# Kernel optimization log

Hardware: AMD Instinct MI355X
Metric: run time of the kernel (lower is better)

## Reference

```python
import jax, jax.numpy as jnp
import numpy as np


def setup_inputs() -> dict:
    key = jax.random.key(0)
    k1, k2, k3 = jax.random.split(key, 3)
    dim = 192
    x = jax.random.normal(k1, (4, dim, 256, 256), dtype=jnp.float32)
    # Conv2d(5*dim, dim, 1): weight [dim, 5*dim], bias [dim]
    W = jax.random.normal(k2, (dim, 5 * dim), dtype=jnp.float32) * 0.02
    b = jax.random.normal(k3, (dim,), dtype=jnp.float32) * 0.02
    return {"x": x, "W": W, "b": b}


def _shifts(x):
    # Matches torch: cat([x,
    #   pad(x[:,:,:,1:], (0,1)),   # take right neighbor (zero at last col)
    #   pad(x[:,:,:,:-1], (1,0)),  # take left neighbor (zero at first col)
    #   pad(x[:,:,1:,:], (0,0,0,1)),  # take below neighbor (zero at last row)
    #   pad(x[:,:,:-1,:], (0,0,1,0))  # take above neighbor (zero at first row)
    # ], dim=1)
    right = jnp.pad(x[:, :, :, 1:], ((0, 0), (0, 0), (0, 0), (0, 1)))
    left = jnp.pad(x[:, :, :, :-1], ((0, 0), (0, 0), (0, 0), (1, 0)))
    down = jnp.pad(x[:, :, 1:, :], ((0, 0), (0, 0), (0, 1), (0, 0)))
    up = jnp.pad(x[:, :, :-1, :], ((0, 0), (0, 0), (1, 0), (0, 0)))
    return jnp.concatenate([x, right, left, down, up], axis=1)  # [B, 5C, H, W]


def reference(x, W, b):
    xs = _shifts(x)  # [B, 5C, H, W]
    # 1x1 conv == per-pixel matmul over channels
    out = jnp.einsum("bchw,oc->bohw", xs, W) + b[None, :, None, None]
    return out
```

## Files before the change

### kernel.cpp

```cpp
#include <hip/hip_runtime.h>
#include <hip/hip_bf16.h>
#include <stdint.h>

#define CDIM 192
#define KDIM 960
#define HW   65536
#define WI   256

#define OFF_W    50331648u
#define OFF_BIAS 50700288u
#define OFF_FLAG 50701056u
#define NEED_TOTAL 50701120u

typedef __attribute__((ext_vector_type(8))) short short8;
typedef __attribute__((ext_vector_type(4))) float floatx4;

__device__ __forceinline__ uint16_t f2b(float v) {
    __hip_bfloat16 h = __float2bfloat16(v);
    return *reinterpret_cast<uint16_t*>(&h);
}

__global__ __launch_bounds__(256) void detect_kernel(const uint32_t* __restrict__ xw,
                                                     int* __restrict__ flag) {
    __shared__ int cnt;
    if (threadIdx.x == 0) cnt = 0;
    __syncthreads();
    int local = 0;
    #pragma unroll
    for (int i = 0; i < 4; ++i) {
        int s = threadIdx.x * 4 + i;
        uint32_t d = xw[(size_t)s * 24571];
        uint32_t e = (d >> 7) & 0xFF;
        if (e >= 110 && e <= 130) ++local;
    }
    atomicAdd(&cnt, local);
    __syncthreads();
    if (threadIdx.x == 0) *flag = (cnt >= 512) ? 1 : 0;
}

__global__ __launch_bounds__(256) void prep_kernel(const void* __restrict__ Wsrc,
                                                   const void* __restrict__ bsrc,
                                                   __hip_bfloat16* __restrict__ Wb,
                                                   float* __restrict__ bfp,
                                                   const int* __restrict__ flag) {
    const int f = *flag;
    if (blockIdx.x < 720) {
        int i = blockIdx.x * 256 + threadIdx.x;
        float v = f ? __bfloat162float(((const __hip_bfloat16*)Wsrc)[i])
                    : ((const float*)Wsrc)[i];
        Wb[i] = __float2bfloat16(v);
    } else if (threadIdx.x < CDIM) {
        int j = threadIdx.x;
        bfp[j] = f ? __bfloat162float(((const __hip_bfloat16*)bsrc)[j])
                   : ((const float*)bsrc)[j];
    }
}

__global__ __launch_bounds__(256) void transpose_kernel(const void* __restrict__ xsrc,
                                                        __hip_bfloat16* __restrict__ xt,
                                                        const int* __restrict__ flag,
                                                        int base_b) {
    __shared__ uint4 lds[1536];
    const int bid = blockIdx.x;
    const int tid = threadIdx.x;
    const int bb = bid >> 10;
    const int b  = base_b + bb;
    const int p0 = (bid & 1023) << 6;
    const int f = *flag;
    if (f) {
        const uint4* xg = (const uint4*)xsrc;
        #pragma unroll
        for (int it = 0; it < 6; ++it) {
            int idx = tid + it * 256;
            int c = idx >> 3, pxc = idx & 7;
            size_t off = (size_t)(b * CDIM + c) * HW + p0 + pxc * 8;
            lds[idx] = xg[off >> 3];
        }
    } else {
        const float4* xg = (const float4*)xsrc;
        #pragma unroll
        for (int it = 0; it < 6; ++it) {
            int idx = tid + it * 256;
            int c = idx >> 3, pxc = idx & 7;
            size_t off4 = ((size_t)(b * CDIM + c) * HW + p0 + pxc * 8) >> 2;
            float4 v0 = xg[off4], v1 = xg[off4 + 1];
            uint32_t w0 = f2b(v0.x) | ((uint32_t)f2b(v0.y) << 16);
            uint32_t w1 = f2b(v0.z) | ((uint32_t)f2b(v0.w) << 16);
            uint32_t w2 = f2b(v1.x) | ((uint32_t)f2b(v1.y) << 16);
            uint32_t w3 = f2b(v1.z) | ((uint32_t)f2b(v1.w) << 16);
            lds[idx] = make_uint4(w0, w1, w2, w3);
        }
    }
    __syncthreads();
    const uint16_t* lu = (const uint16_t*)lds;
    #pragma unroll
    for (int it = 0; it < 6; ++it) {
        int idx = tid + it * 256;
        int px = idx & 63, cc = idx >> 6;
        uint32_t d[4];
        #pragma unroll
        for (int w = 0; w < 4; ++w) {
            uint32_t lo = lu[(cc * 8 + 2 * w) * 64 + px];
            uint32_t hi = lu[(cc * 8 + 2 * w + 1) * 64 + px];
            d[w] = lo | (hi << 16);
        }
        size_t row = (size_t)bb * HW + p0 + px;
        *(uint4*)(xt + row * CDIM + cc * 8) = make_uint4(d[0], d[1], d[2], d[3]);
    }
}

__device__ __forceinline__ void gload16(const void* g, void* l) {
    __builtin_amdgcn_global_load_lds(
        (const __attribute__((address_space(1))) uint32_t*)g,
        (__attribute__((address_space(3))) uint32_t*)l, 16, 0, 0);
}

__global__ __launch_bounds__(256, 2) void gemm_kernel(const __hip_bfloat16* __restrict__ xt,
                                                      const __hip_bfloat16* __restrict__ Wm,
                                                      const float* __restrict__ biasf,
                                                      void* __restrict__ outv,
                                                      const int* __restrict__ flag,
                                                      int base_b) {
    __shared__ char ldsW[2 * 12288];
    const int f = *flag;
    const int tid  = threadIdx.x;
    const int lane = tid & 63, wave = tid >> 6;
    const int quad = lane >> 4, l15 = lane & 15;
    const int bid = blockIdx.x;
    const int bb = bid >> 9;
    const int b  = base_b + bb;
    const int r  = bid & 511;
    const int h  = r >> 1;
    const int w0 = (r & 1) << 7;
    const int p0 = h * WI + w0;
    const int obase = (wave >> 1) * 96;
    const int nbase = (wave & 1) * 64;

    const char* gw[3];
    int ldsoff[3];
    #pragma unroll
    for (int t = 0; t < 3; ++t) {
        int chunk = tid + t * 256;
        int kq = chunk / 192, o = chunk % 192;
        gw[t] = (const char*)Wm + ((size_t)o * KDIM + kq * 8) * 2;
        ldsoff[t] = chunk * 16;
    }
    int aoff[6];
    #pragma unroll
    for (int mt = 0; mt < 6; ++mt) {
        int o = obase + mt * 16 + l15;
        aoff[mt] = (quad * 192 + o) * 16;
    }
    const char* xb = (const char*)(xt + (size_t)bb * HW * CDIM);
    int prow[4]; bool w255[4], wzero[4];
    #pragma unroll
    for (int nt = 0; nt < 4; ++nt) {
        int pl = nbase + nt * 16 + l15;
        prow[nt]  = p0 + pl;
        w255[nt]  = ((w0 + pl) == 255);
        wzero[nt] = ((w0 + pl) == 0);
    }

    floatx4 acc[6][4];
    #pragma unroll
    for (int mt = 0; mt < 6; ++mt)
        #pragma unroll
        for (int nt = 0; nt < 4; ++nt)
            acc[mt][nt] = (floatx4){0.f, 0.f, 0.f, 0.f};

    #pragma unroll
    for (int t = 0; t < 3; ++t) gload16(gw[t], ldsW + ldsoff[t]);

    for (int s = 0; s < 5; ++s) {
        const int dp = (s == 0) ? 0 : (s == 1) ? 1 : (s == 2) ? -1 : (s == 3) ? WI : -WI;
        const bool skip = (s == 3 && h == 255) || (s == 4 && h == 0);
        const int dpe = skip ? 0 : dp;
        #pragma unroll
        for (int j6 = 0; j6 < 6; ++j6) {
            const int step = s * 6 + j6;
            __syncthreads();
            const int cur = (step & 1) * 12288;
            if (step < 29) {
                const int nxt = ((step + 1) & 1) * 12288;
                #pragma unroll
                for (int t = 0; t < 3; ++t)
                    gload16(gw[t] + (size_t)(step + 1) * 64, ldsW + nxt + ldsoff[t]);
            }
            short8 af[6];
            #pragma unroll
            for (int mt = 0; mt < 6; ++mt)
                af[mt] = *(const short8*)(ldsW + cur + aoff[mt]);
            short8 bf[4];
            #pragma unroll
            for (int nt = 0; nt < 4; ++nt) {
                const bool edge = (s == 1 && w255[nt]) || (s == 2 && wzero[nt]);
                int rowi = prow[nt] + dpe;
                if (edge) rowi = prow[nt];
                short8 v = *(const short8*)(xb +
                    ((size_t)rowi * CDIM + j6 * 32 + quad * 8) * 2);
                if (edge || skip)
                    v = (short8){0, 0, 0, 0, 0, 0, 0, 0};
                bf[nt] = v;
            }
            #pragma unroll
            for (int mt = 0; mt < 6; ++mt)
                #pragma unroll
                for (int nt = 0; nt < 4; ++nt)
                    acc[mt][nt] = __builtin_amdgcn_mfma_f32_16x16x32_bf16(
                        af[mt], bf[nt], acc[mt][nt], 0, 0, 0);
        }
    }

    #pragma unroll
    for (int mt = 0; mt < 6; ++mt) {
        int o0 = obase + mt * 16 + quad * 4;
        float bv[4];
        #pragma unroll
        for (int rr = 0; rr < 4; ++rr) bv[rr] = biasf[o0 + rr];
        #pragma unroll
        for (int nt = 0; nt < 4; ++nt) {
            int px = nbase + nt * 16 + l15;
            size_t base = ((size_t)(b * CDIM + o0) * HW) + p0 + px;
            if (f) {
                __hip_bfloat16* out = (__hip_bfloat16*)outv;
                #pragma unroll
                for (int rr = 0; rr < 4; ++rr)
                    out[base + (size_t)rr * HW] = __float2bfloat16(acc[mt][nt][rr] + bv[rr]);
            } else {
                float* out = (float*)outv;
                #pragma unroll
                for (int rr = 0; rr < 4; ++rr)
                    out[base + (size_t)rr * HW] = acc[mt][nt][rr] + bv[rr];
            }
        }
    }
}

__global__ __launch_bounds__(256) void fallback_kernel(const void* __restrict__ xv,
                                                       const void* __restrict__ Wv,
                                                       const void* __restrict__ bv,
                                                       void* __restrict__ outv,
                                                       const int* __restrict__ flag) {
    __shared__ float Wl[KDIM];
    const int f = *flag;
    const int tid = threadIdx.x;
    const int bid = blockIdx.x;
    const int h = bid & 255;
    const int bo = bid >> 8;
    const int o = bo % CDIM;
    const int b = bo / CDIM;
    if (f) {
        const __hip_bfloat16* W16 = (const __hip_bfloat16*)Wv;
        for (int i = tid; i < KDIM; i += 256) Wl[i] = __bfloat162float(W16[(size_t)o * KDIM + i]);
    } else {
        const float* W32 = (const float*)Wv;
        for (int i = tid; i < KDIM; i += 256) Wl[i] = W32[(size_t)o * KDIM + i];
    }
    __syncthreads();
    const size_t pb = (size_t)b * CDIM * HW + (size_t)h * WI + tid;
    float acc = f ? __bfloat162float(((const __hip_bfloat16*)bv)[o]) : ((const float*)bv)[o];
    if (f) {
        const __hip_bfloat16* x = (const __hip_bfloat16*)xv;
        for (int c = 0; c < CDIM; ++c) {
            const __hip_bfloat16* xp = x + pb + (size_t)c * HW;
            float ctr = __bfloat162float(xp[0]);
            float rgt = (tid < 255) ? __bfloat162float(xp[1])   : 0.f;
            float lft = (tid > 0)   ? __bfloat162float(xp[-1])  : 0.f;
            float dwn = (h < 255)   ? __bfloat162float(xp[WI])  : 0.f;
            float up  = (h > 0)     ? __bfloat162float(xp[-WI]) : 0.f;
            acc += ctr * Wl[c] + rgt * Wl[192 + c] + lft * Wl[384 + c]
                 + dwn * Wl[576 + c] + up * Wl[768 + c];
        }
    } else {
        const float* x = (const float*)xv;
        for (int c = 0; c < CDIM; ++c) {
            const float* xp = x + pb + (size_t)c * HW;
            float ctr = xp[0];
            float rgt = (tid < 255) ? xp[1]   : 0.f;
            float lft = (tid > 0)   ? xp[-1]  : 0.f;
            float dwn = (h < 255)   ? xp[WI]  : 0.f;
            float up  = (h > 0)     ? xp[-WI] : 0.f;
            acc += ctr * Wl[c] + rgt * Wl[192 + c] + lft * Wl[384 + c]
                 + dwn * Wl[576 + c] + up * Wl[768 + c];
        }
    }
    size_t oidx = (size_t)bo * HW + (size_t)h * WI + tid;
    if (f) ((__hip_bfloat16*)outv)[oidx] = __float2bfloat16(acc);
    else   ((float*)outv)[oidx] = acc;
}

extern "C" void kernel_launch(void* const* d_in, const int* in_sizes, int n_in,
                              void* d_out, int out_size, void* d_ws, size_t ws_size,
                              hipStream_t stream) {
    const uint32_t* xw = (const uint32_t*)d_in[0];
    char* ws = (char*)d_ws;

    if (ws_size >= NEED_TOTAL) {
        int* flag = (int*)(ws + OFF_FLAG);
        __hip_bfloat16* xt = (__hip_bfloat16*)ws;
        __hip_bfloat16* Wb = (__hip_bfloat16*)(ws + OFF_W);
        float* bfp = (float*)(ws + OFF_BIAS);
        detect_kernel<<<1, 256, 0, stream>>>(xw, flag);
        prep_kernel<<<721, 256, 0, stream>>>(d_in[1], d_in[2], Wb, bfp, flag);
        for (int rnd = 0; rnd < 2; ++rnd) {
            transpose_kernel<<<2048, 256, 0, stream>>>(d_in[0], xt, flag, 2 * rnd);
            gemm_kernel<<<1024, 256, 0, stream>>>(xt, Wb, bfp, d_out, flag, 2 * rnd);
        }
    } else {
        int* flag = (int*)ws;
        detect_kernel<<<1, 256, 0, stream>>>(xw, flag);
        fallback_kernel<<<4 * CDIM * 256, 256, 0, stream>>>(d_in[0], d_in[1], d_in[2],
                                                            d_out, flag);
    }
}
```

Baseline: 573.6 us.

## Fuse transpose into GEMM by staging shifted input rows in LDS

Removes the separate transpose kernel and the bf16 transposed workspace. The fused kernel loads three input rows (h-1, h, h+1) for each 32-channel slice straight from the original NCHW tensor, converts them to bf16 and stores them in LDS with halo columns. The five shifted operands are then read from LDS, so input is fetched once per slice instead of five times from global memory. It also remaps workgroup IDs, adds explicit waitcnt/barrier scheduling and raises priority around the MFMA block. The cost is extra LDS use and per-slice synchronisation, plus strided global loads of 2 bytes per element in the staging step.

```diff
diff --git a/kernel.cpp b/kernel.cpp
--- a/kernel.cpp
+++ b/kernel.cpp
@@ -7,10 +7,14 @@
 #define HW   65536
 #define WI   256
 
-#define OFF_W    50331648u
-#define OFF_BIAS 50700288u
-#define OFF_FLAG 50701056u
-#define NEED_TOTAL 50701120u
+#define OFF_BIAS 368640u
+#define OFF_FLAG 369408u
+#define NEED_WS  369472u
+
+#define ROW_B    80
+#define SLICE_B  10560
+#define WOFF     31680
+#define WBUF     12288
 
 typedef __attribute__((ext_vector_type(8))) short short8;
 typedef __attribute__((ext_vector_type(4))) float floatx4;
@@ -56,80 +60,31 @@
     }
 }
 
-__global__ __launch_bounds__(256) void transpose_kernel(const void* __restrict__ xsrc,
-                                                        __hip_bfloat16* __restrict__ xt,
-                                                        const int* __restrict__ flag,
-                                                        int base_b) {
-    __shared__ uint4 lds[1536];
-    const int bid = blockIdx.x;
-    const int tid = threadIdx.x;
-    const int bb = bid >> 10;
-    const int b  = base_b + bb;
-    const int p0 = (bid & 1023) << 6;
-    const int f = *flag;
-    if (f) {
-        const uint4* xg = (const uint4*)xsrc;
-        #pragma unroll
-        for (int it = 0; it < 6; ++it) {
-            int idx = tid + it * 256;
-            int c = idx >> 3, pxc = idx & 7;
-            size_t off = (size_t)(b * CDIM + c) * HW + p0 + pxc * 8;
-            lds[idx] = xg[off >> 3];
-        }
-    } else {
-        const float4* xg = (const float4*)xsrc;
-        #pragma unroll
-        for (int it = 0; it < 6; ++it) {
-            int idx = tid + it * 256;
-            int c = idx >> 3, pxc = idx & 7;
-            size_t off4 = ((size_t)(b * CDIM + c) * HW + p0 + pxc * 8) >> 2;
-            float4 v0 = xg[off4], v1 = xg[off4 + 1];
-            uint32_t w0 = f2b(v0.x) | ((uint32_t)f2b(v0.y) << 16);
-            uint32_t w1 = f2b(v0.z) | ((uint32_t)f2b(v0.w) << 16);
-            uint32_t w2 = f2b(v1.x) | ((uint32_t)f2b(v1.y) << 16);
-            uint32_t w3 = f2b(v1.z) | ((uint32_t)f2b(v1.w) << 16);
-            lds[idx] = make_uint4(w0, w1, w2, w3);
-        }
-    }
-    __syncthreads();
-    const uint16_t* lu = (const uint16_t*)lds;
-    #pragma unroll
-    for (int it = 0; it < 6; ++it) {
-        int idx = tid + it * 256;
-        int px = idx & 63, cc = idx >> 6;
-        uint32_t d[4];
-        #pragma unroll
-        for (int w = 0; w < 4; ++w) {
-            uint32_t lo = lu[(cc * 8 + 2 * w) * 64 + px];
-            uint32_t hi = lu[(cc * 8 + 2 * w + 1) * 64 + px];
-            d[w] = lo | (hi << 16);
-        }
-        size_t row = (size_t)bb * HW + p0 + px;
-        *(uint4*)(xt + row * CDIM + cc * 8) = make_uint4(d[0], d[1], d[2], d[3]);
-    }
-}
-
 __device__ __forceinline__ void gload16(const void* g, void* l) {
     __builtin_amdgcn_global_load_lds(
         (const __attribute__((address_space(1))) uint32_t*)g,
         (__attribute__((address_space(3))) uint32_t*)l, 16, 0, 0);
 }
 
-__global__ __launch_bounds__(256, 2) void gemm_kernel(const __hip_bfloat16* __restrict__ xt,
-                                                      const __hip_bfloat16* __restrict__ Wm,
-                                                      const float* __restrict__ biasf,
-                                                      void* __restrict__ outv,
-                                                      const int* __restrict__ flag,
-                                                      int base_b) {
-    __shared__ char ldsW[2 * 12288];
+__global__ __launch_bounds__(256, 2) void fused_kernel(const void* __restrict__ xsrc,
+                                                       const __hip_bfloat16* __restrict__ Wm,
+                                                       const float* __restrict__ biasf,
+                                                       void* __restrict__ outv,
+                                                       const int* __restrict__ flag) {
+    __shared__ char lds[WOFF + 2 * WBUF];
+    char* xsl  = lds;
+    char* ldsW = lds + WOFF;
     const int f = *flag;
     const int tid  = threadIdx.x;
     const int lane = tid & 63, wave = tid >> 6;
     const int quad = lane >> 4, l15 = lane & 15;
-    const int bid = blockIdx.x;
-    const int bb = bid >> 9;
-    const int b  = base_b + bb;
-    const int r  = bid & 511;
+
+    const int nwg  = (int)gridDim.x;
+    const int bid0 = (int)blockIdx.x;
+    const int wg   = (bid0 & 7) * (nwg >> 3) + (bid0 >> 3);
+
+    const int bb = wg >> 9;
+    const int r  = wg & 511;
     const int h  = r >> 1;
     const int w0 = (r & 1) << 7;
     const int p0 = h * WI + w0;
@@ -151,14 +106,33 @@
         int o = obase + mt * 16 + l15;
         aoff[mt] = (quad * 192 + o) * 16;
     }
-    const char* xb = (const char*)(xt + (size_t)bb * HW * CDIM);
-    int prow[4]; bool w255[4], wzero[4];
+
+    int pxa[4]; bool w255[4], wzero[4];
     #pragma unroll
     for (int nt = 0; nt < 4; ++nt) {
         int pl = nbase + nt * 16 + l15;
-        prow[nt]  = p0 + pl;
+        pxa[nt]   = (pl + 1) * ROW_B;
         w255[nt]  = ((w0 + pl) == 255);
         wzero[nt] = ((w0 + pl) == 0);
+    }
+
+    const int scc  = tid >> 7;
+    const int spx  = (tid & 127) + 1;
+    const int scol = w0 + (tid & 127);
+    const int ec = tid >> 1, ee = tid & 1;
+    int ecol = ee ? (w0 + 128) : (w0 - 1);
+    if (ecol < 0) ecol = 0;
+    if (ecol > 255) ecol = 255;
+    const int epx = ee ? 129 : 0;
+
+    const size_t esz = f ? 2u : 4u;
+    const char* xp = (const char*)xsrc + (size_t)bb * CDIM * HW * esz;
+
+    int hr[3];
+    #pragma unroll
+    for (int rr = 0; rr < 3; ++rr) {
+        int v = h - 1 + rr;
+        hr[rr] = v < 0 ? 0 : (v > 255 ? 255 : v);
     }
 
     floatx4 acc[6][4];
@@ -168,46 +142,100 @@
         for (int nt = 0; nt < 4; ++nt)
             acc[mt][nt] = (floatx4){0.f, 0.f, 0.f, 0.f};
 
+#define STAGE(JJ)                                                                          \
+    {                                                                                      \
+        const int c0 = (JJ) * 32;                                                          \
+        _Pragma("unroll")                                                                  \
+        for (int rr = 0; rr < 3; ++rr) {                                                   \
+            uint32_t tmp[16];                                                              \
+            const size_t rowoff = (size_t)hr[rr] * WI;                                     \
+            if (f) {                                                                       \
+                const uint16_t* xg = (const uint16_t*)xp;                                  \
+                _Pragma("unroll")                                                          \
+                for (int cc = 0; cc < 16; ++cc)                                            \
+                    tmp[cc] = xg[(size_t)(c0 + scc * 16 + cc) * HW + rowoff + scol];       \
+            } else {                                                                       \
+                const float* xg = (const float*)xp;                                        \
+                _Pragma("unroll")                                                          \
+                for (int cc = 0; cc < 16; ++cc)                                            \
+                    tmp[cc] = f2b(xg[(size_t)(c0 + scc * 16 + cc) * HW + rowoff + scol]);  \
+            }                                                                              \
+            uint4 q0, q1;                                                                  \
+            q0.x = tmp[0] | (tmp[1] << 16);  q0.y = tmp[2] | (tmp[3] << 16);               \
+            q0.z = tmp[4] | (tmp[5] << 16);  q0.w = tmp[6] | (tmp[7] << 16);               \
+            q1.x = tmp[8] | (tmp[9] << 16);  q1.y = tmp[10] | (tmp[11] << 16);             \
+            q1.z = tmp[12] | (tmp[13] << 16); q1.w = tmp[14] | (tmp[15] << 16);            \
+            char* base = xsl + rr * SLICE_B + spx * ROW_B + scc * 32;                      \
+            *(uint4*)(base)      = q0;                                                     \
+            *(uint4*)(base + 16) = q1;                                                     \
+        }                                                                                  \
+        if (tid < 64) {                                                                    \
+            _Pragma("unroll")                                                              \
+            for (int rr = 0; rr < 3; ++rr) {                                               \
+                const size_t gi = (size_t)(c0 + ec) * HW + (size_t)hr[rr] * WI + ecol;     \
+                uint16_t v = f ? ((const uint16_t*)xp)[gi]                                 \
+                               : f2b(((const float*)xp)[gi]);                              \
+                *(uint16_t*)(xsl + rr * SLICE_B + epx * ROW_B + ec * 2) = v;               \
+            }                                                                              \
+        }                                                                                  \
+    }
+
     #pragma unroll
     for (int t = 0; t < 3; ++t) gload16(gw[t], ldsW + ldsoff[t]);
-
-    for (int s = 0; s < 5; ++s) {
-        const int dp = (s == 0) ? 0 : (s == 1) ? 1 : (s == 2) ? -1 : (s == 3) ? WI : -WI;
-        const bool skip = (s == 3 && h == 255) || (s == 4 && h == 0);
-        const int dpe = skip ? 0 : dp;
+    STAGE(0)
+    __syncthreads();
+
+    for (int j = 0; j < 6; ++j) {
         #pragma unroll
-        for (int j6 = 0; j6 < 6; ++j6) {
-            const int step = s * 6 + j6;
-            __syncthreads();
-            const int cur = (step & 1) * 12288;
-            if (step < 29) {
-                const int nxt = ((step + 1) & 1) * 12288;
+        for (int s = 0; s < 5; ++s) {
+            const int cur = (s & 1) * WBUF;
+            __builtin_amdgcn_s_barrier();
+            __builtin_amdgcn_sched_barrier(0);
+            if (s < 4) {
+                const int nxt = WBUF - cur;
                 #pragma unroll
                 for (int t = 0; t < 3; ++t)
-                    gload16(gw[t] + (size_t)(step + 1) * 64, ldsW + nxt + ldsoff[t]);
+                    gload16(gw[t] + (size_t)((s + 1) * 6 + j) * 64, ldsW + nxt + ldsoff[t]);
             }
+            __builtin_amdgcn_sched_barrier(0);
+            if (s < 4) asm volatile("s_waitcnt vmcnt(3)" ::: "memory");
+            else       asm volatile("s_waitcnt vmcnt(0)" ::: "memory");
+            __builtin_amdgcn_sched_barrier(0);
+            __builtin_amdgcn_s_barrier();
+            __builtin_amdgcn_sched_barrier(0);
+
             short8 af[6];
             #pragma unroll
             for (int mt = 0; mt < 6; ++mt)
                 af[mt] = *(const short8*)(ldsW + cur + aoff[mt]);
+
+            const int so   = (s == 3) ? 2 * SLICE_B : (s == 4) ? 0 : SLICE_B;
+            const int dw80 = (s == 1) ? ROW_B : (s == 2) ? -ROW_B : 0;
+            const bool skip = (s == 3 && h == 255) || (s == 4 && h == 0);
             short8 bf[4];
             #pragma unroll
             for (int nt = 0; nt < 4; ++nt) {
-                const bool edge = (s == 1 && w255[nt]) || (s == 2 && wzero[nt]);
-                int rowi = prow[nt] + dpe;
-                if (edge) rowi = prow[nt];
-                short8 v = *(const short8*)(xb +
-                    ((size_t)rowi * CDIM + j6 * 32 + quad * 8) * 2);
-                if (edge || skip)
-                    v = (short8){0, 0, 0, 0, 0, 0, 0, 0};
-                bf[nt] = v;
+                short8 v = *(const short8*)(xsl + so + pxa[nt] + dw80 + quad * 16);
+                const bool kill = skip || (s == 1 && w255[nt]) || (s == 2 && wzero[nt]);
+                bf[nt] = kill ? (short8){0, 0, 0, 0, 0, 0, 0, 0} : v;
             }
+
+            __builtin_amdgcn_s_setprio(1);
             #pragma unroll
             for (int mt = 0; mt < 6; ++mt)
                 #pragma unroll
                 for (int nt = 0; nt < 4; ++nt)
                     acc[mt][nt] = __builtin_amdgcn_mfma_f32_16x16x32_bf16(
                         af[mt], bf[nt], acc[mt][nt], 0, 0, 0);
+            __builtin_amdgcn_s_setprio(0);
+        }
+        if (j < 5) {
+            __syncthreads();
+            #pragma unroll
+            for (int t = 0; t < 3; ++t)
+                gload16(gw[t] + (size_t)(j + 1) * 64, ldsW + ldsoff[t]);
+            STAGE(j + 1)
+            __syncthreads();
         }
     }
 
@@ -220,7 +248,7 @@
         #pragma unroll
         for (int nt = 0; nt < 4; ++nt) {
             int px = nbase + nt * 16 + l15;
-            size_t base = ((size_t)(b * CDIM + o0) * HW) + p0 + px;
+            size_t base = ((size_t)(bb * CDIM + o0) * HW) + p0 + px;
             if (f) {
                 __hip_bfloat16* out = (__hip_bfloat16*)outv;
                 #pragma unroll
@@ -234,6 +262,7 @@
             }
         }
     }
+#undef STAGE
 }
 
 __global__ __launch_bounds__(256) void fallback_kernel(const void* __restrict__ xv,
@@ -295,17 +324,13 @@
     const uint32_t* xw = (const uint32_t*)d_in[0];
     char* ws = (char*)d_ws;
 
-    if (ws_size >= NEED_TOTAL) {
-        int* flag = (int*)(ws + OFF_FLAG);
-        __hip_bfloat16* xt = (__hip_bfloat16*)ws;
-        __hip_bfloat16* Wb = (__hip_bfloat16*)(ws + OFF_W);
+    if (ws_size >= NEED_WS) {
+        __hip_bfloat16* Wb = (__hip_bfloat16*)ws;
         float* bfp = (float*)(ws + OFF_BIAS);
+        int* flag  = (int*)(ws + OFF_FLAG);
         detect_kernel<<<1, 256, 0, stream>>>(xw, flag);
         prep_kernel<<<721, 256, 0, stream>>>(d_in[1], d_in[2], Wb, bfp, flag);
-        for (int rnd = 0; rnd < 2; ++rnd) {
-            transpose_kernel<<<2048, 256, 0, stream>>>(d_in[0], xt, flag, 2 * rnd);
-            gemm_kernel<<<1024, 256, 0, stream>>>(xt, Wb, bfp, d_out, flag, 2 * rnd);
-        }
+        fused_kernel<<<2048, 256, 0, stream>>>(d_in[0], Wb, bfp, d_out, flag);
     } else {
         int* flag = (int*)ws;
         detect_kernel<<<1, 256, 0, stream>>>(xw, flag);
```

After: 464.0 us. -19.1%, faster.
